# Kernel tuning notes

Measured on AMD Instinct MI355X. Metric: run time of the kernel, lower is better.

Reference implementation:

```python
import jax, jax.numpy as jnp
import numpy as np

# Hyperparameters from __init__ defaults / chosen init kwargs
GAMMA_NEG = 4.0
GAMMA_POS = 1.0
CLIP = 0.05
EPS = 1e-8
ALPHA1 = 2.0
ALPHA_OTHER = 0.5
TOP_K = 10

B, C = 2048, 9605


def setup_inputs() -> dict:
    key = jax.random.key(0)
    k_x, k_y, k_c, k_r, k_d, k_o = jax.random.split(key, 6)
    x = jax.random.normal(k_x, (B, C), dtype=jnp.float32)
    y = (jax.random.uniform(k_y, (B, C)) < 0.01).astype(jnp.float32)
    compost_idx = jax.random.randint(k_c, (30,), 0, C, dtype=jnp.int32)
    recycle_idx = jax.random.randint(k_r, (70,), 0, C, dtype=jnp.int32)
    donate_idx = jax.random.randint(k_d, (70,), 0, C, dtype=jnp.int32)
    other_idx = jax.random.randint(k_o, (40,), 0, C, dtype=jnp.int32)
    # dense whitelist mapping: 0 = not in W_human mapping; priority compost>recycle>donate
    wl_map = jnp.zeros((C,), dtype=jnp.int32)
    wl_map = wl_map.at[other_idx].set(4)
    wl_map = wl_map.at[donate_idx].set(3)
    wl_map = wl_map.at[recycle_idx].set(2)
    wl_map = wl_map.at[compost_idx].set(1)
    return {"x": x, "y": y, "compost_idx": compost_idx,
            "recycle_idx": recycle_idx, "donate_idx": donate_idx,
            "wl_map": wl_map}


def reference(x, y, compost_idx, recycle_idx, donate_idx, wl_map):
    b, c = x.shape
    xs_pos = jax.nn.sigmoid(x)
    xs_neg = jnp.minimum(1.0 - xs_pos + CLIP, 1.0)  # clip shift, clamp max=1
    # base asymmetric BCE term: y*log(p) + (1-y)*log(1-p+clip)
    base = (y * jnp.log(jnp.maximum(xs_pos, EPS))
            + (1.0 - y) * jnp.log(jnp.maximum(xs_neg, EPS)))  # [B, C]

    # per-sample ground-truth whitelist groups (find_gt_whitelist)
    has1 = jnp.sum(y[:, compost_idx], axis=1) > 0  # [B]
    has2 = jnp.sum(y[:, recycle_idx], axis=1) > 0
    has3 = jnp.sum(y[:, donate_idx], axis=1) > 0
    gt_only4 = ~(has1 | has2 | has3)  # gt_whitelist == [4]

    # top-10 predicted classes (argsort descending, first 10)
    _, top_idx = jax.lax.top_k(xs_pos, TOP_K)  # [B, 10]
    rows = jnp.arange(b)

    def step(carry, j):
        # j: [B] class index at current rank; sequential over rank (order matters)
        mult, found = carry
        wl = wl_map[j]                      # group id of this class, 0 if unmapped
        in_map = wl > 0
        in_gt = (((wl == 1) & has1) | ((wl == 2) & has2)
                 | ((wl == 3) & has3) | ((wl == 4) & gt_only4))
        f = jnp.where(in_map & gt_only4, ALPHA_OTHER, 1.0)
        f = f * jnp.where(in_map & (~in_gt) & (~found), ALPHA1, 1.0)
        mult = mult.at[rows, j].multiply(f)
        found = found | (in_map & in_gt)
        return (mult, found), None

    init = (jnp.ones((b, c), x.dtype), jnp.zeros((b,), dtype=bool))
    (mult, found), _ = jax.lax.scan(step, init, top_idx.T)  # scan over 10 ranks

    # if no gt-whitelist match found in top-10: multiply all top-10 by alpha1 again
    extra = jnp.where(found[:, None], 1.0, ALPHA1)  # [B, 1]
    mult = mult.at[rows[:, None], top_idx].multiply(
        jnp.broadcast_to(extra, (b, TOP_K)))

    # asymmetric focal weighting (computed without grad in original)
    pt = xs_pos * y + xs_neg * (1.0 - y)
    gamma = GAMMA_POS * y + GAMMA_NEG * (1.0 - y)
    w = jax.lax.stop_gradient(jnp.power(1.0 - pt, gamma))

    return -jnp.sum(base * mult * w)
```

## Files before the change

### kernel.cpp

```cpp
#include <hip/hip_runtime.h>

#define TOPK 10
#define CLIP 0.05f
#define EPSV 1e-8f
#define ALPHA1 2.0f
#define ALPHA_OTHER 0.5f
#define TCAND 2.5f
#define MAXC 512

__device__ __forceinline__ unsigned long long pack_vc(float v, int c, int C) {
  unsigned u = __float_as_uint(v);
  unsigned key = (u & 0x80000000u) ? ~u : (u | 0x80000000u);
  return ((unsigned long long)key << 32) | (unsigned)(C - c);
}
__device__ __forceinline__ float unpack_v(unsigned long long p) {
  unsigned key = (unsigned)(p >> 32);
  unsigned u = (key & 0x80000000u) ? (key & 0x7fffffffu) : ~key;
  return __uint_as_float(u);
}
__device__ __forceinline__ int unpack_c(unsigned long long p, int C) {
  return C - (int)(unsigned)(p & 0xffffffffu);
}

__device__ __forceinline__ float base_w(float xv, bool pos) {
  float p = 1.f / (1.f + __expf(-xv));
  float xneg = fminf(1.f - p + CLIP, 1.f);
  float q = pos ? p : xneg;
  float b = __logf(fmaxf(q, EPSV));
  float t = 1.f - q;
  float t2 = t * t;
  float w = pos ? t : t2 * t2;
  return b * w;
}

__device__ __forceinline__ void proc4(float4 X, float4 Y, float4& acc,
                                      unsigned& cmask, int slot) {
  acc.x += base_w(X.x, Y.x > 0.5f);
  acc.y += base_w(X.y, Y.y > 0.5f);
  acc.z += base_w(X.z, Y.z > 0.5f);
  acc.w += base_w(X.w, Y.w > 0.5f);
  float mx = fmaxf(fmaxf(X.x, X.y), fmaxf(X.z, X.w));
  cmask |= (mx > TCAND ? 1u : 0u) << slot;
}

__global__ __launch_bounds__(256) void asl_kernel(
    const float* __restrict__ x, const float* __restrict__ y,
    const int* __restrict__ compost, const int* __restrict__ recycle,
    const int* __restrict__ donate, const int* __restrict__ wl_map,
    float* __restrict__ out, int C, int n1, int n2, int n3)
{
  const int row = blockIdx.x;
  const float* xr = x + (size_t)row * (size_t)C;
  const float* yr = y + (size_t)row * (size_t)C;
  const int tid = threadIdx.x;
  const int lane = tid & 63;
  const int wave = tid >> 6;

  __shared__ int s_has[3];
  __shared__ unsigned s_cnt;
  __shared__ unsigned long long s_cand[MAXC];
  __shared__ float s_sum[4];
  __shared__ unsigned long long s_top[TOPK];

  if (tid < 3) s_has[tid] = 0;
  if (tid == 0) s_cnt = 0;
  __syncthreads();

  const int ntot = n1 + n2 + n3;
  float gflag = 0.f; int gwhich = -1;
  if (tid < ntot) {
    int colI;
    if (tid < n1)           { gwhich = 0; colI = compost[tid]; }
    else if (tid < n1 + n2) { gwhich = 1; colI = recycle[tid - n1]; }
    else                    { gwhich = 2; colI = donate[tid - n1 - n2]; }
    gflag = yr[colI];
  }

  float ssc = 0.f;

#define PUSH(V, CCOL)                                                     \
  do {                                                                    \
    unsigned _i = atomicAdd(&s_cnt, 1u);                                  \
    if (_i < MAXC) s_cand[_i] = pack_vc((V), (CCOL), C);                  \
  } while (0)
#define PROC_DIRECT(XV, YV, COL)                                          \
  do {                                                                    \
    float _xv = (XV);                                                     \
    ssc += base_w(_xv, (YV) > 0.5f);                                      \
    if (_xv > TCAND) PUSH(_xv, (COL));                                    \
  } while (0)

  int lead = (int)((4u - ((unsigned)((size_t)row * (size_t)C) & 3u)) & 3u);
  if (lead > C) lead = C;
  for (int col = tid; col < lead; col += 256) PROC_DIRECT(xr[col], yr[col], col);

  const int nvec = (C - lead) >> 2;
  const float4* __restrict__ x4 = (const float4*)(xr + lead);
  const float4* __restrict__ y4 = (const float4*)(yr + lead);

  float4 sacc = make_float4(0.f, 0.f, 0.f, 0.f);
  unsigned cmask = 0;

  int slotbase = 0;
  for (int base = tid; base < nvec; base += 1024, slotbase += 4) {
    const bool v1 = base + 256 < nvec;
    const bool v2 = base + 512 < nvec;
    const bool v3 = base + 768 < nvec;
    float4 xv0, xv1, xv2, xv3, yv0, yv1, yv2, yv3;
    xv0 = x4[base];                 yv0 = y4[base];
    if (v1) { xv1 = x4[base + 256]; yv1 = y4[base + 256]; }
    if (v2) { xv2 = x4[base + 512]; yv2 = y4[base + 512]; }
    if (v3) { xv3 = x4[base + 768]; yv3 = y4[base + 768]; }
    proc4(xv0, yv0, sacc, cmask, slotbase + 0);
    if (v1) proc4(xv1, yv1, sacc, cmask, slotbase + 1);
    if (v2) proc4(xv2, yv2, sacc, cmask, slotbase + 2);
    if (v3) proc4(xv3, yv3, sacc, cmask, slotbase + 3);
  }

  for (int col = lead + nvec * 4 + tid; col < C; col += 256)
    PROC_DIRECT(xr[col], yr[col], col);

  if (gwhich >= 0 && gflag > 0.5f) s_has[gwhich] = 1;
  for (int i = 256 + tid; i < ntot; i += 256) {
    int which, colI;
    if (i < n1)           { which = 0; colI = compost[i]; }
    else if (i < n1 + n2) { which = 1; colI = recycle[i - n1]; }
    else                  { which = 2; colI = donate[i - n1 - n2]; }
    if (yr[colI] > 0.5f) s_has[which] = 1;
  }

  while (cmask) {
    int b = __ffs(cmask) - 1;
    cmask &= cmask - 1;
    int o = b >> 2, j = b & 3;
    int i = tid + o * 1024 + j * 256;
    float4 X = x4[i];
    int cb = lead + i * 4;
    if (X.x > TCAND) PUSH(X.x, cb + 0);
    if (X.y > TCAND) PUSH(X.y, cb + 1);
    if (X.z > TCAND) PUSH(X.z, cb + 2);
    if (X.w > TCAND) PUSH(X.w, cb + 3);
  }
#undef PROC_DIRECT
#undef PUSH

  float sum = ssc + sacc.x + sacc.y + sacc.z + sacc.w;
#pragma unroll
  for (int off = 32; off > 0; off >>= 1) sum += __shfl_xor(sum, off, 64);
  if (lane == 0) s_sum[wave] = sum;
  __syncthreads();

  if (wave == 0) {
    const unsigned cnt = s_cnt;
    unsigned long long ls[TOPK];
#pragma unroll
    for (int s = 0; s < TOPK; s++) ls[s] = 0ULL;

#define INSERT(P)                                                          \
    do {                                                                   \
      unsigned long long _p = (P);                                         \
      if (_p > ls[TOPK - 1]) {                                             \
        _Pragma("unroll")                                                  \
        for (int _s = 0; _s < TOPK; _s++) {                                \
          bool _g = _p > ls[_s];                                           \
          unsigned long long _t = _g ? ls[_s] : _p;                        \
          ls[_s] = _g ? _p : ls[_s];                                       \
          _p = _t;                                                         \
        }                                                                  \
      }                                                                    \
    } while (0)

    if (cnt >= TOPK && cnt <= MAXC) {
      for (unsigned i = lane; i < cnt; i += 64) INSERT(s_cand[i]);
    } else {
      for (int col = lane; col < C; col += 64) INSERT(pack_vc(xr[col], col, C));
    }
#undef INSERT

    for (int r = 0; r < TOPK; r++) {
      unsigned long long mine = ls[0];
      unsigned long long best = mine;
#pragma unroll
      for (int off = 32; off > 0; off >>= 1) {
        unsigned long long o = __shfl_xor(best, off, 64);
        best = (o > best) ? o : best;
      }
      if (lane == 0) s_top[r] = best;
      if (mine == best) {
#pragma unroll
        for (int s = 0; s < TOPK - 1; s++) ls[s] = ls[s + 1];
        ls[TOPK - 1] = 0ULL;
      }
    }
  }
  __syncthreads();

  if (tid == 0) {
    float total = s_sum[0] + s_sum[1] + s_sum[2] + s_sum[3];
    const bool h1 = s_has[0] != 0, h2 = s_has[1] != 0, h3 = s_has[2] != 0;
    const bool gt4 = !(h1 || h2 || h3);

    bool found = false;
    float fr[TOPK];
#pragma unroll
    for (int r = 0; r < TOPK; r++) {
      int col = unpack_c(s_top[r], C);
      int wl = wl_map[col];
      bool in_map = wl > 0;
      bool in_gt = (wl == 1 && h1) || (wl == 2 && h2) ||
                   (wl == 3 && h3) || (wl == 4 && gt4);
      float f = 1.f;
      if (in_map && gt4) f *= ALPHA_OTHER;
      if (in_map && !in_gt && !found) f *= ALPHA1;
      fr[r] = f;
      found = found || (in_map && in_gt);
    }
    const float extra = found ? 1.f : ALPHA1;
#pragma unroll
    for (int r = 0; r < TOPK; r++) {
      float mult = fr[r] * extra;
      if (mult != 1.f) {
        int col = unpack_c(s_top[r], C);
        float xv = unpack_v(s_top[r]);
        float bwv = base_w(xv, yr[col] > 0.5f);
        total += (mult - 1.f) * bwv;
      }
    }
    atomicAdd(out, -total);
  }
}

extern "C" void kernel_launch(void* const* d_in, const int* in_sizes, int n_in,
                              void* d_out, int out_size, void* d_ws, size_t ws_size,
                              hipStream_t stream) {
  const float* x       = (const float*)d_in[0];
  const float* y       = (const float*)d_in[1];
  const int*   compost = (const int*)d_in[2];
  const int*   recycle = (const int*)d_in[3];
  const int*   donate  = (const int*)d_in[4];
  const int*   wl_map  = (const int*)d_in[5];
  float* out = (float*)d_out;

  const int C  = in_sizes[5];
  const int B  = in_sizes[0] / C;
  const int n1 = in_sizes[2], n2 = in_sizes[3], n3 = in_sizes[4];

  hipMemsetAsync(out, 0, sizeof(float), stream);
  asl_kernel<<<B, 256, 0, stream>>>(x, y, compost, recycle, donate, wl_map,
                                    out, C, n1, n2, n3);
}
```

Baseline: 207.5 us.

## Split into flat grid-stride streaming pass plus per-row candidate top-k kernel

Replaces the one-block-per-row kernel with a flat grid-stride streaming kernel. It computes the focal-weighted loss over the whole tensor and pushes elements above a threshold into per-row candidate buffers in workspace through atomics. A second small kernel, one wave per row, takes the top-10 from those candidates (falling back to a full row scan) and applies the whitelist multiplier corrections. The aim is better load balance and memory streaming across the whole tensor. In exchange it adds global atomics, an extra launch and memset, and depends on workspace size. The old path remains as a fallback.

```diff
diff --git a/kernel.cpp b/kernel.cpp
--- a/kernel.cpp
+++ b/kernel.cpp
@@ -6,6 +6,7 @@
 #define ALPHA1 2.0f
 #define ALPHA_OTHER 0.5f
 #define TCAND 2.5f
+#define SLOTS 128
 #define MAXC 512
 
 __device__ __forceinline__ unsigned long long pack_vc(float v, int c, int C) {
@@ -42,6 +43,193 @@
   float mx = fmaxf(fmaxf(X.x, X.y), fmaxf(X.z, X.w));
   cmask |= (mx > TCAND ? 1u : 0u) << slot;
 }
+
+
+__device__ __forceinline__ void push_cand(unsigned e, float v, int C,
+                                          unsigned* cnt,
+                                          unsigned long long* cand) {
+  unsigned row = e / (unsigned)C;
+  int col = (int)(e - row * (unsigned)C);
+  unsigned i = atomicAdd(&cnt[row], 1u);
+  if (i < SLOTS) cand[(size_t)row * SLOTS + i] = pack_vc(v, col, C);
+}
+
+__global__ __launch_bounds__(256) void stream_kernel(
+    const float* __restrict__ x, const float* __restrict__ y,
+    float* __restrict__ out, unsigned* __restrict__ cnt,
+    unsigned long long* __restrict__ cand, int C, unsigned total)
+{
+  const int tid = threadIdx.x;
+  const unsigned nth = gridDim.x * 256u;
+  const unsigned gtid = blockIdx.x * 256u + tid;
+  const unsigned n4 = total >> 2;
+  const float4* __restrict__ x4 = (const float4*)x;
+  const float4* __restrict__ y4 = (const float4*)y;
+
+  float4 sacc = make_float4(0.f, 0.f, 0.f, 0.f);
+  float ssc = 0.f;
+  unsigned cmask = 0;
+
+  int slotbase = 0;
+  for (unsigned base = gtid; base < n4; base += 4u * nth, slotbase += 4) {
+    const bool v1 = base + nth < n4;
+    const bool v2 = base + 2u * nth < n4;
+    const bool v3 = base + 3u * nth < n4;
+    float4 xv0, xv1, xv2, xv3, yv0, yv1, yv2, yv3;
+    xv0 = x4[base];                  yv0 = y4[base];
+    if (v1) { xv1 = x4[base + nth];      yv1 = y4[base + nth]; }
+    if (v2) { xv2 = x4[base + 2u * nth]; yv2 = y4[base + 2u * nth]; }
+    if (v3) { xv3 = x4[base + 3u * nth]; yv3 = y4[base + 3u * nth]; }
+    if (slotbase <= 28) {
+      proc4(xv0, yv0, sacc, cmask, slotbase + 0);
+      if (v1) proc4(xv1, yv1, sacc, cmask, slotbase + 1);
+      if (v2) proc4(xv2, yv2, sacc, cmask, slotbase + 2);
+      if (v3) proc4(xv3, yv3, sacc, cmask, slotbase + 3);
+    } else {
+      float4 X[4] = {xv0, xv1, xv2, xv3};
+      float4 Y[4] = {yv0, yv1, yv2, yv3};
+      bool vv[4] = {true, v1, v2, v3};
+#pragma unroll
+      for (int k = 0; k < 4; k++) {
+        if (!vv[k]) break;
+        sacc.x += base_w(X[k].x, Y[k].x > 0.5f);
+        sacc.y += base_w(X[k].y, Y[k].y > 0.5f);
+        sacc.z += base_w(X[k].z, Y[k].z > 0.5f);
+        sacc.w += base_w(X[k].w, Y[k].w > 0.5f);
+        unsigned e = (base + (unsigned)k * nth) * 4u;
+        if (X[k].x > TCAND) push_cand(e + 0, X[k].x, C, cnt, cand);
+        if (X[k].y > TCAND) push_cand(e + 1, X[k].y, C, cnt, cand);
+        if (X[k].z > TCAND) push_cand(e + 2, X[k].z, C, cnt, cand);
+        if (X[k].w > TCAND) push_cand(e + 3, X[k].w, C, cnt, cand);
+      }
+    }
+  }
+
+  for (unsigned i = (n4 << 2) + gtid; i < total; i += nth) {
+    float xv = x[i];
+    ssc += base_w(xv, y[i] > 0.5f);
+    if (xv > TCAND) push_cand(i, xv, C, cnt, cand);
+  }
+
+  while (cmask) {
+    int b = __ffs(cmask) - 1;
+    cmask &= cmask - 1;
+    unsigned i4 = gtid + (unsigned)b * nth;
+    float4 X = x4[i4];
+    unsigned e = i4 * 4u;
+    if (X.x > TCAND) push_cand(e + 0, X.x, C, cnt, cand);
+    if (X.y > TCAND) push_cand(e + 1, X.y, C, cnt, cand);
+    if (X.z > TCAND) push_cand(e + 2, X.z, C, cnt, cand);
+    if (X.w > TCAND) push_cand(e + 3, X.w, C, cnt, cand);
+  }
+
+  float sum = ssc + sacc.x + sacc.y + sacc.z + sacc.w;
+#pragma unroll
+  for (int off = 32; off > 0; off >>= 1) sum += __shfl_xor(sum, off, 64);
+  __shared__ float s_sum[4];
+  const int lane = tid & 63, wave = tid >> 6;
+  if (lane == 0) s_sum[wave] = sum;
+  __syncthreads();
+  if (tid == 0) atomicAdd(out, -(s_sum[0] + s_sum[1] + s_sum[2] + s_sum[3]));
+}
+
+__global__ __launch_bounds__(64) void topk_kernel(
+    const float* __restrict__ x, const float* __restrict__ y,
+    const int* __restrict__ compost, const int* __restrict__ recycle,
+    const int* __restrict__ donate, const int* __restrict__ wl_map,
+    float* __restrict__ out, const unsigned* __restrict__ cnt,
+    const unsigned long long* __restrict__ cand,
+    int C, int n1, int n2, int n3)
+{
+  const int row = blockIdx.x;
+  const int lane = threadIdx.x;
+  const float* __restrict__ xr = x + (size_t)row * (size_t)C;
+  const float* __restrict__ yr = y + (size_t)row * (size_t)C;
+
+  const int ntot = n1 + n2 + n3;
+  bool f1 = false, f2 = false, f3 = false;
+  for (int i = lane; i < ntot; i += 64) {
+    int colI;
+    if (i < n1)           { colI = compost[i];           if (yr[colI] > 0.5f) f1 = true; }
+    else if (i < n1 + n2) { colI = recycle[i - n1];      if (yr[colI] > 0.5f) f2 = true; }
+    else                  { colI = donate[i - n1 - n2];  if (yr[colI] > 0.5f) f3 = true; }
+  }
+  const bool h1 = __ballot(f1) != 0ULL;
+  const bool h2 = __ballot(f2) != 0ULL;
+  const bool h3 = __ballot(f3) != 0ULL;
+  const bool gt4 = !(h1 || h2 || h3);
+
+  const unsigned c = cnt[row];
+  unsigned long long ls[TOPK];
+#pragma unroll
+  for (int s = 0; s < TOPK; s++) ls[s] = 0ULL;
+
+#define INSERT(P)                                                          \
+  do {                                                                     \
+    unsigned long long _p = (P);                                           \
+    if (_p > ls[TOPK - 1]) {                                               \
+      _Pragma("unroll")                                                    \
+      for (int _s = 0; _s < TOPK; _s++) {                                  \
+        bool _g = _p > ls[_s];                                             \
+        unsigned long long _t = _g ? ls[_s] : _p;                          \
+        ls[_s] = _g ? _p : ls[_s];                                         \
+        _p = _t;                                                           \
+      }                                                                    \
+    }                                                                      \
+  } while (0)
+
+  if (c >= TOPK && c <= SLOTS) {
+    const unsigned long long* cr = cand + (size_t)row * SLOTS;
+    for (unsigned i = lane; i < c; i += 64) INSERT(cr[i]);
+  } else {
+    for (int col = lane; col < C; col += 64) INSERT(pack_vc(xr[col], col, C));
+  }
+#undef INSERT
+
+  unsigned long long myTop = 0ULL;
+  for (int r = 0; r < TOPK; r++) {
+    unsigned long long mine = ls[0];
+    unsigned long long best = mine;
+#pragma unroll
+    for (int off = 32; off > 0; off >>= 1) {
+      unsigned long long o = __shfl_xor(best, off, 64);
+      best = (o > best) ? o : best;
+    }
+    if (lane == r) myTop = best;
+    if (mine == best) {
+#pragma unroll
+      for (int s = 0; s < TOPK - 1; s++) ls[s] = ls[s + 1];
+      ls[TOPK - 1] = 0ULL;
+    }
+  }
+
+  const bool valid = (lane < TOPK) && (myTop != 0ULL);
+  int col = 0; float val = 0.f; int wl = 0;
+  if (valid) {
+    col = unpack_c(myTop, C);
+    val = unpack_v(myTop);
+    wl = wl_map[col];
+  }
+  const bool in_map = valid && (wl > 0);
+  const bool in_gt = in_map && ((wl == 1 && h1) || (wl == 2 && h2) ||
+                                (wl == 3 && h3) || (wl == 4 && gt4));
+  const unsigned long long mm = __ballot(in_map && in_gt);
+  const bool foundbefore = (mm & ((1ULL << lane) - 1ULL)) != 0ULL;
+  float f = 1.f;
+  if (in_map && gt4) f *= ALPHA_OTHER;
+  if (in_map && !in_gt && !foundbefore) f *= ALPHA1;
+  const float extra = (mm != 0ULL) ? 1.f : ALPHA1;
+
+  float corr = 0.f;
+  if (valid) {
+    float mult = f * extra;
+    if (mult != 1.f) corr = (mult - 1.f) * base_w(val, yr[col] > 0.5f);
+  }
+#pragma unroll
+  for (int off = 32; off > 0; off >>= 1) corr += __shfl_xor(corr, off, 64);
+  if (lane == 0 && corr != 0.f) atomicAdd(out, -corr);
+}
+
 
 __global__ __launch_bounds__(256) void asl_kernel(
     const float* __restrict__ x, const float* __restrict__ y,
@@ -246,6 +434,28 @@
   const int n1 = in_sizes[2], n2 = in_sizes[3], n3 = in_sizes[4];
 
   hipMemsetAsync(out, 0, sizeof(float), stream);
-  asl_kernel<<<B, 256, 0, stream>>>(x, y, compost, recycle, donate, wl_map,
-                                    out, C, n1, n2, n3);
-}
+
+  const size_t cntBytes = (size_t)B * 4;
+  const size_t candOff  = (cntBytes + 15) & ~(size_t)15;
+  const size_t need     = candOff + (size_t)B * SLOTS * 8;
+
+  if (d_ws != nullptr && ws_size >= need) {
+    unsigned* cnt = (unsigned*)d_ws;
+    unsigned long long* cand = (unsigned long long*)((char*)d_ws + candOff);
+    hipMemsetAsync(cnt, 0, cntBytes, stream);
+
+    const size_t totalS = (size_t)B * (size_t)C;
+    const unsigned total = (unsigned)totalS;
+    size_t n4s = totalS / 4;
+    int nblk = (int)((n4s + 255) / 256);
+    if (nblk > 2048) nblk = 2048;
+    if (nblk < 1) nblk = 1;
+
+    stream_kernel<<<nblk, 256, 0, stream>>>(x, y, out, cnt, cand, C, total);
+    topk_kernel<<<B, 64, 0, stream>>>(x, y, compost, recycle, donate, wl_map,
+                                      out, cnt, cand, C, n1, n2, n3);
+  } else {
+    asl_kernel<<<B, 256, 0, stream>>>(x, y, compost, recycle, donate, wl_map,
+                                      out, C, n1, n2, n3);
+  }
+}
```

Measured after the change: 247.5 us. 1.19x slower.
